# Kernel tuning notes

Measured on AMD Instinct MI355X. Metric: run time of the kernel, lower is better.

The kernel has to match this reference:

```python
import jax, jax.numpy as jnp
import numpy as np

C = 256      # channels (multiple of 32 for GroupNorm)
K = 3        # kernel
PAD = 1      # padding
G = 32       # GroupNorm groups
EPS = 1e-5


def setup_inputs() -> dict:
    key = jax.random.key(0)
    ks = jax.random.split(key, 7)
    B, H, W = 4, 64, 64
    return {
        "x": jax.random.normal(ks[0], (B, C, H, W), jnp.float32),
        "offset": jax.random.normal(ks[1], (B, 2 * K * K, H, W), jnp.float32),
        "weight": jax.random.normal(ks[2], (C, C, K, K), jnp.float32) * 0.01,
        "att_w": jax.random.normal(ks[3], (1, C), jnp.float32) * 0.01,
        "att_b": jnp.zeros((1,), jnp.float32),
        "gamma": jnp.ones((C,), jnp.float32),
        "beta": jnp.zeros((C,), jnp.float32),
    }


def _bilinear_one(xb, py, px):
    # xb: [C, H, W]; py, px: [KK, H, W] fractional sample coords (zero-pad outside)
    H, W = xb.shape[1], xb.shape[2]
    y0 = jnp.floor(py)
    x0 = jnp.floor(px)
    y1 = y0 + 1.0
    x1 = x0 + 1.0
    wy1 = py - y0
    wy0 = 1.0 - wy1
    wx1 = px - x0
    wx0 = 1.0 - wx1

    def g(yi, xi):
        valid = (yi >= 0) & (yi < H) & (xi >= 0) & (xi < W)
        yc = jnp.clip(yi, 0, H - 1).astype(jnp.int32)
        xc = jnp.clip(xi, 0, W - 1).astype(jnp.int32)
        return xb[:, yc, xc] * valid[None].astype(xb.dtype)  # [C, KK, H, W]

    return (g(y0, x0) * (wy0 * wx0)[None] + g(y0, x1) * (wy0 * wx1)[None]
            + g(y1, x0) * (wy1 * wx0)[None] + g(y1, x1) * (wy1 * wx1)[None])


def reference(x, offset, weight, att_w, att_b, gamma, beta):
    B, Cc, H, W = x.shape
    KK = K * K
    off = offset.reshape(B, KK, 2, H, W)  # (dy, dx) per kernel tap
    ii, jj = jnp.meshgrid(jnp.arange(K), jnp.arange(K), indexing='ij')
    dky = (ii - PAD).reshape(KK).astype(x.dtype)
    dkx = (jj - PAD).reshape(KK).astype(x.dtype)
    ys = jnp.arange(H, dtype=x.dtype)
    xs = jnp.arange(W, dtype=x.dtype)
    # sample coords [B, KK, H, W]
    py = ys[None, :, None] + dky[:, None, None] + off[:, :, 0]
    px = xs[None, None, :] + dkx[:, None, None] + off[:, :, 1]

    # deformable unfold: [B, C, KK, H, W]
    xu = jax.vmap(_bilinear_one)(x, py, px)

    # max over kernel taps -> channel attention gate
    xm = xu.max(axis=2)  # [B, C, H, W]
    att = jax.nn.sigmoid(jnp.einsum('bchw,oc->bohw', xm, att_w)
                         + att_b[None, :, None, None])  # [B, 1, H, W]

    # gate the unfolded samples, then emulate the conv as one GEMM
    xw = xu * att[:, :, None]  # broadcast over C, KK
    cols = xw.transpose(1, 2, 0, 3, 4).reshape(Cc * KK, B * H * W)  # [C*KK, BHW]
    out = (weight.reshape(Cc, Cc * KK) @ cols).reshape(Cc, B, H, W).transpose(1, 0, 2, 3)

    # GroupNorm(32, C) + ReLU
    og = out.reshape(B, G, Cc // G, H, W)
    mu = og.mean(axis=(2, 3, 4), keepdims=True)
    var = og.var(axis=(2, 3, 4), keepdims=True)
    on = ((og - mu) * jax.lax.rsqrt(var + EPS)).reshape(B, Cc, H, W)
    return jax.nn.relu(on * gamma[None, :, None, None] + beta[None, :, None, None])
```

## Files before the change

### kernel.cpp

```cpp
#include <hip/hip_runtime.h>

#define CT 256
#define KDIM 2304
#define COLP 296
#define CCOL (32 * COLP)
#define XSP 4608

typedef unsigned short u16;
typedef _Float16 h2 __attribute__((ext_vector_type(2)));
typedef _Float16 h8 __attribute__((ext_vector_type(8)));
typedef __attribute__((ext_vector_type(4))) float f32x4;

__device__ __forceinline__ unsigned pkh(float a, float b) {
    h2 r; r[0] = (_Float16)a; r[1] = (_Float16)b;
    return __builtin_bit_cast(unsigned, r);
}

__device__ __forceinline__ void gload_lds16(const uint4* g, u16* l) {
    __builtin_amdgcn_global_load_lds((const __attribute__((address_space(1))) void*)g,
                                     (__attribute__((address_space(3))) void*)l, 16, 0, 0);
}

__global__ __launch_bounds__(256) void k_prep(const float* __restrict__ x, uint4* __restrict__ xi,
                                              const float* __restrict__ wgt, uint4* __restrict__ pw)
{
    if (blockIdx.x < 2048) {
        int u = blockIdx.x * 256 + threadIdx.x;
        int bcg = u >> 12, p = u & 4095;
        const float* xp = x + (((size_t)bcg) << 15) + p;
        unsigned r[4];
#pragma unroll
        for (int i = 0; i < 4; ++i)
            r[i] = pkh(xp[(size_t)(2 * i) << 12], xp[(size_t)(2 * i + 1) << 12]);
        uint4 o; o.x = r[0]; o.y = r[1]; o.z = r[2]; o.w = r[3];
        xi[u] = o;
    } else {
        int u = (blockIdx.x - 2048) * 256 + threadIdx.x;
        int kc = u >> 10, rm = u & 1023;
        int m = rm >> 2, j = rm & 3;
        int round = kc / 9, tap = kc - round * 9;
        const float* src = wgt + (size_t)m * KDIM + tap;
        int c0 = round * 32 + j * 8;
        unsigned q[4];
#pragma unroll
        for (int i = 0; i < 4; ++i)
            q[i] = pkh(src[(size_t)(c0 + 2 * i) * 9], src[(size_t)(c0 + 2 * i + 1) * 9]);
        uint4 o; o.x = q[0]; o.y = q[1]; o.z = q[2]; o.w = q[3];
        pw[u] = o;
    }
}

__device__ __forceinline__ void gather_one(int it2, int sp, int xsb, size_t gfall,
                                           const uint2* s_wt, const int2* s_off,
                                           const u16* Xs, u16* col,
                                           const uint4* __restrict__ xi, int rbase, int nw)
{
    int tap = it2 >> 5, nn = it2 & 31;
    uint2 wp = s_wt[it2];
    h2 w01 = __builtin_bit_cast(h2, wp.x);
    h2 w23 = __builtin_bit_cast(h2, wp.y);
    h2 wxp = (h2){w01[0], w01[0]}, wyp = (h2){w01[1], w01[1]};
    h2 wzp = (h2){w23[0], w23[0]}, wwp = (h2){w23[1], w23[1]};
    int2 of = s_off[it2];
    int P00 = of.x & 0xffff, P01 = (of.x >> 16) & 0xffff;
    int P10 = of.y & 0xffff, P11 = (of.y >> 16) & 0xffff;
    uint4 c00, c01, c10, c11;
    int Q;
    Q = P00 - rbase;
    if ((unsigned)Q < (unsigned)nw) c00 = *(const uint4*)&Xs[xsb + Q * 8]; else c00 = xi[gfall + P00];
    Q = P01 - rbase;
    if ((unsigned)Q < (unsigned)nw) c01 = *(const uint4*)&Xs[xsb + Q * 8]; else c01 = xi[gfall + P01];
    Q = P10 - rbase;
    if ((unsigned)Q < (unsigned)nw) c10 = *(const uint4*)&Xs[xsb + Q * 8]; else c10 = xi[gfall + P10];
    Q = P11 - rbase;
    if ((unsigned)Q < (unsigned)nw) c11 = *(const uint4*)&Xs[xsb + Q * 8]; else c11 = xi[gfall + P11];
    const unsigned* a00 = (const unsigned*)&c00;
    const unsigned* a01 = (const unsigned*)&c01;
    const unsigned* a10 = (const unsigned*)&c10;
    const unsigned* a11 = (const unsigned*)&c11;
    unsigned o[4];
#pragma unroll
    for (int q = 0; q < 4; ++q) {
        h2 r = wxp * __builtin_bit_cast(h2, a00[q]) + wyp * __builtin_bit_cast(h2, a01[q])
             + wzp * __builtin_bit_cast(h2, a10[q]) + wwp * __builtin_bit_cast(h2, a11[q]);
        o[q] = __builtin_bit_cast(unsigned, r);
    }
    uint4 ov; ov.x = o[0]; ov.y = o[1]; ov.z = o[2]; ov.w = o[3];
    *(uint4*)&col[nn * COLP + tap * 32 + sp * 8] = ov;
}

__global__ __launch_bounds__(512, 2) void k_main(const uint4* __restrict__ xi, const float* __restrict__ off,
                                                 const uint4* __restrict__ pw, const float* __restrict__ att_w,
                                                 const float* __restrict__ att_b,
                                                 float* __restrict__ outp, float* __restrict__ gnpart)
{
    __shared__ uint2 s_wt[288];
    __shared__ int2 s_off[288];
    __shared__ u16 Xs[4 * XSP];
    __shared__ u16 col[2 * CCOL];
    __shared__ float s_att[32];

    int bid = blockIdx.x;
    int xcd = bid & 7, idx = bid >> 3;
    int b = xcd >> 1;
    int local = ((xcd & 1) << 6) + idx;
    int h = local >> 1, half = local & 1;
    int lbid = b * 128 + local;
    int n0 = half * 32;

    int tid = threadIdx.x;
    int lane = tid & 63, w = tid >> 6;
    int l15 = lane & 15, kb = lane >> 4;
    int wm = w * 32;
    int nn_a = w * 4 + (lane >> 4);
    int ca = (lane & 15) * 2;

    for (int e = tid; e < 288; e += 512) {
        int kk = e >> 5, wl = e & 31;
        int ww_ = n0 + wl;
        int ky = kk / 3, kx = kk - ky * 3;
        float dy = off[((size_t)(b * 18 + 2 * kk) * 64 + h) * 64 + ww_];
        float dx = off[((size_t)(b * 18 + 2 * kk + 1) * 64 + h) * 64 + ww_];
        float py = (float)(h + ky - 1) + dy;
        float px = (float)(ww_ + kx - 1) + dx;
        float y0f = floorf(py), x0f = floorf(px);
        int y0 = (int)y0f, x0 = (int)x0f;
        float fy = py - y0f, fx = px - x0f;
        float vy0 = (y0 >= 0 && y0 < 64) ? 1.f : 0.f;
        float vy1 = (y0 >= -1 && y0 < 63) ? 1.f : 0.f;
        float vx0 = (x0 >= 0 && x0 < 64) ? 1.f : 0.f;
        float vx1 = (x0 >= -1 && x0 < 63) ? 1.f : 0.f;
        float w0 = (1.f - fy) * (1.f - fx) * vy0 * vx0;
        float w1 = (1.f - fy) * fx * vy0 * vx1;
        float w2 = fy * (1.f - fx) * vy1 * vx0;
        float w3 = fy * fx * vy1 * vx1;
        uint2 wp;
        wp.x = pkh(w0, w1);
        wp.y = pkh(w2, w3);
        int yc0 = min(max(y0, 0), 63), yc1 = min(max(y0 + 1, 0), 63);
        int xc0 = min(max(x0, 0), 63), xc1 = min(max(x0 + 1, 0), 63);
        s_wt[e] = wp;
        s_off[e] = make_int2((yc0 * 64 + xc0) | ((yc0 * 64 + xc1) << 16),
                             (yc1 * 64 + xc0) | ((yc1 * 64 + xc1) << 16));
    }

    int r0c = max(0, h - 4), r1c = min(63, h + 4);
    int nrows = r1c - r0c + 1, nw = nrows * 64, rbase = r0c * 64;
    size_t xib = (size_t)(b * 32) << 12;

    float att_acc = 0.f;
    f32x4 acc[2][2];
#pragma unroll
    for (int mt = 0; mt < 2; ++mt)
#pragma unroll
        for (int nt = 0; nt < 2; ++nt) acc[mt][nt] = (f32x4){0.f, 0.f, 0.f, 0.f};

    int pwoff[2];
#pragma unroll
    for (int mt = 0; mt < 2; ++mt) pwoff[mt] = (wm + mt * 16 + l15) * 4 + kb;

#pragma unroll
    for (int cgl = 0; cgl < 2; ++cgl)
        for (int e = tid; e < nw; e += 512)
            gload_lds16(&xi[xib + ((size_t)cgl << 12) + rbase + e], &Xs[(cgl * XSP + e * 8)]);

    for (int stage = 0; stage < 16; ++stage) {
        int buf = stage & 1;
        __syncthreads();
        if (stage < 15) {
            size_t nb = xib + ((size_t)((stage + 1) * 2) << 12) + rbase;
#pragma unroll
            for (int cgl = 0; cgl < 2; ++cgl)
                for (int e = tid; e < nw; e += 512)
                    gload_lds16(&xi[nb + ((size_t)cgl << 12) + e],
                                &Xs[(((buf ^ 1) * 2 + cgl) * XSP + e * 8)]);
        }

        if (stage >= 2 && !(stage & 1)) {
            int rr = (stage >> 1) - 1;
            const u16* cb = col + (rr & 1) * CCOL;

            uint4 aa[4][2];
#pragma unroll
            for (int ts = 0; ts < 4; ++ts)
#pragma unroll
                for (int mt = 0; mt < 2; ++mt)
                    aa[ts][mt] = pw[(size_t)(rr * 9 + ts) * 1024 + pwoff[mt]];

            {
                int sp = ca >> 3, co = ca & 7;
                const u16* base = &cb[nn_a * COLP + sp * 8 + co];
                float m0 = -1e30f, m1 = -1e30f;
#pragma unroll
                for (int t = 0; t < 9; ++t) {
                    unsigned v = *(const unsigned*)(base + t * 32);
                    h2 vv = __builtin_bit_cast(h2, v);
                    m0 = fmaxf(m0, (float)vv[0]);
                    m1 = fmaxf(m1, (float)vv[1]);
                }
                int cbx = rr * 32 + ca;
                att_acc += att_w[cbx] * m0 + att_w[cbx + 1] * m1;
            }

#pragma unroll
            for (int ts = 0; ts < 9; ++ts) {
                h8 bf[2];
#pragma unroll
                for (int nt = 0; nt < 2; ++nt)
                    bf[nt] = *(const h8*)&cb[(nt * 16 + l15) * COLP + ts * 32 + kb * 8];
                h8 af[2];
#pragma unroll
                for (int mt = 0; mt < 2; ++mt) af[mt] = __builtin_bit_cast(h8, aa[ts & 3][mt]);
                if (ts + 4 < 9) {
#pragma unroll
                    for (int mt = 0; mt < 2; ++mt)
                        aa[ts & 3][mt] = pw[(size_t)(rr * 9 + ts + 4) * 1024 + pwoff[mt]];
                }
#pragma unroll
                for (int mt = 0; mt < 2; ++mt)
#pragma unroll
                    for (int nt = 0; nt < 2; ++nt)
                        acc[mt][nt] = __builtin_amdgcn_mfma_f32_16x16x32_f16(af[mt], bf[nt], acc[mt][nt], 0, 0, 0);
            }
        }

        {
            u16* cw = col + ((stage >> 1) & 1) * CCOL;
            int it = tid;
            int cgl = (it >= 288) ? 1 : 0;
            gather_one(it - cgl * 288, buf * 2 + cgl, (buf * 2 + cgl) * XSP,
                       xib + ((size_t)(stage * 2 + cgl) << 12), s_wt, s_off, Xs, cw, xi, rbase, nw);
            if (tid >= 448) {
                int it2 = tid + 64;
                gather_one(it2 - 288, buf * 2 + 1, (buf * 2 + 1) * XSP,
                           xib + ((size_t)(stage * 2 + 1) << 12), s_wt, s_off, Xs, cw, xi, rbase, nw);
            }
        }
    }

    __syncthreads();
    {
        int rr = 7;
        const u16* cb = col + (rr & 1) * CCOL;
        uint4 aa[4][2];
#pragma unroll
        for (int ts = 0; ts < 4; ++ts)
#pragma unroll
            for (int mt = 0; mt < 2; ++mt)
                aa[ts][mt] = pw[(size_t)(rr * 9 + ts) * 1024 + pwoff[mt]];
        {
            int sp = ca >> 3, co = ca & 7;
            const u16* base = &cb[nn_a * COLP + sp * 8 + co];
            float m0 = -1e30f, m1 = -1e30f;
#pragma unroll
            for (int t = 0; t < 9; ++t) {
                unsigned v = *(const unsigned*)(base + t * 32);
                h2 vv = __builtin_bit_cast(h2, v);
                m0 = fmaxf(m0, (float)vv[0]);
                m1 = fmaxf(m1, (float)vv[1]);
            }
            int cbx = rr * 32 + ca;
            att_acc += att_w[cbx] * m0 + att_w[cbx + 1] * m1;
        }
#pragma unroll
        for (int ts = 0; ts < 9; ++ts) {
            h8 bf[2];
#pragma unroll
            for (int nt = 0; nt < 2; ++nt)
                bf[nt] = *(const h8*)&cb[(nt * 16 + l15) * COLP + ts * 32 + kb * 8];
            h8 af[2];
#pragma unroll
            for (int mt = 0; mt < 2; ++mt) af[mt] = __builtin_bit_cast(h8, aa[ts & 3][mt]);
            if (ts + 4 < 9) {
#pragma unroll
                for (int mt = 0; mt < 2; ++mt)
                    aa[ts & 3][mt] = pw[(size_t)(rr * 9 + ts + 4) * 1024 + pwoff[mt]];
            }
#pragma unroll
            for (int mt = 0; mt < 2; ++mt)
#pragma unroll
                for (int nt = 0; nt < 2; ++nt)
                    acc[mt][nt] = __builtin_amdgcn_mfma_f32_16x16x32_f16(af[mt], bf[nt], acc[mt][nt], 0, 0, 0);
        }
    }

#pragma unroll
    for (int d = 1; d <= 8; d <<= 1) att_acc += __shfl_xor(att_acc, d);
    if ((lane & 15) == 0) s_att[nn_a] = 1.f / (1.f + expf(-(att_acc + att_b[0])));
    __syncthreads();

    float attn[2];
#pragma unroll
    for (int nt = 0; nt < 2; ++nt) attn[nt] = s_att[nt * 16 + l15];

#pragma unroll
    for (int mt = 0; mt < 2; ++mt) {
        float s1 = 0.f, s2 = 0.f;
#pragma unroll
        for (int nt = 0; nt < 2; ++nt)
#pragma unroll
            for (int r = 0; r < 4; ++r) {
                float v = acc[mt][nt][r] * attn[nt];
                int m = wm + mt * 16 + kb * 4 + r;
                outp[(((size_t)(b * CT + m)) << 12) + h * 64 + n0 + nt * 16 + l15] = v;
                s1 += v; s2 += v * v;
            }
#pragma unroll
        for (int d = 1; d <= 16; d <<= 1) {
            s1 += __shfl_xor(s1, d);
            s2 += __shfl_xor(s2, d);
        }
        if ((lane & 31) == 0) {
            int gidx = w * 4 + mt * 2 + (kb >> 1);
            gnpart[lbid * 64 + gidx * 2] = s1;
            gnpart[lbid * 64 + gidx * 2 + 1] = s2;
        }
    }
}

__global__ __launch_bounds__(256) void k_gn(const float* __restrict__ gnpart, const float* __restrict__ gamma,
                                            const float* __restrict__ beta, float* __restrict__ outp)
{
    __shared__ float rs1[128], rs2[128];
    __shared__ float s_stat[2];
    int bg = blockIdx.x;
    int b = bg >> 5, g = bg & 31;
    int tid = threadIdx.x;
    if (tid < 128) {
        int blk = (b * 64 + (tid >> 1)) * 2 + (tid & 1);
        rs1[tid] = gnpart[blk * 64 + g * 2];
        rs2[tid] = gnpart[blk * 64 + g * 2 + 1];
    }
    __syncthreads();
    if (tid < 64) {
        float a = rs1[tid] + rs1[tid + 64];
        float c = rs2[tid] + rs2[tid + 64];
#pragma unroll
        for (int d = 1; d <= 32; d <<= 1) {
            a += __shfl_xor(a, d);
            c += __shfl_xor(c, d);
        }
        if (tid == 0) {
            float mean = a * (1.f / 32768.f);
            float var = c * (1.f / 32768.f) - mean * mean;
            s_stat[0] = mean;
            s_stat[1] = rsqrtf(var + 1e-5f);
        }
    }
    __syncthreads();
    float mean = s_stat[0], rstd = s_stat[1];
    float4* p4 = (float4*)(outp + ((size_t)(b * CT + g * 8) << 12));
    for (int i = tid; i < 8192; i += 256) {
        int c = g * 8 + (i >> 10);
        float ga = gamma[c], be = beta[c];
        float4 v = p4[i];
        float4 r;
        r.x = fmaxf((v.x - mean) * rstd * ga + be, 0.f);
        r.y = fmaxf((v.y - mean) * rstd * ga + be, 0.f);
        r.z = fmaxf((v.z - mean) * rstd * ga + be, 0.f);
        r.w = fmaxf((v.w - mean) * rstd * ga + be, 0.f);
        p4[i] = r;
    }
}

extern "C" void kernel_launch(void* const* d_in, const int* in_sizes, int n_in,
                              void* d_out, int out_size, void* d_ws, size_t ws_size,
                              hipStream_t stream)
{
    const float* x = (const float*)d_in[0];
    const float* off = (const float*)d_in[1];
    const float* wgt = (const float*)d_in[2];
    const float* attw = (const float*)d_in[3];
    const float* attb = (const float*)d_in[4];
    const float* gamma = (const float*)d_in[5];
    const float* beta = (const float*)d_in[6];
    float* outp = (float*)d_out;

    char* ws = (char*)d_ws;
    uint4* xi = (uint4*)ws;
    uint4* pw = (uint4*)(ws + 8388608);
    float* gnpart = (float*)(ws + 9568256);

    k_prep<<<dim3(2336), dim3(256), 0, stream>>>(x, xi, wgt, pw);
    k_main<<<dim3(512), dim3(512), 0, stream>>>(xi, off, pw, attw, attb, outp, gnpart);
    k_gn<<<dim3(128), dim3(256), 0, stream>>>(gnpart, gamma, beta, outp);
}
```

Before: 146.0 us.

## Fuse prep, main and GroupNorm into one cooperative kernel with grid syncs

```diff
diff --git a/kernel.cpp b/kernel.cpp
--- a/kernel.cpp
+++ b/kernel.cpp
@@ -1,10 +1,14 @@
 #include <hip/hip_runtime.h>
+#include <hip/hip_cooperative_groups.h>
+
+namespace cg = cooperative_groups;
 
 #define CT 256
 #define KDIM 2304
 #define COLP 296
 #define CCOL (32 * COLP)
-#define XSP 4608
+#define XSPB 4608
+#define XSPF 3584
 
 typedef unsigned short u16;
 typedef _Float16 h2 __attribute__((ext_vector_type(2)));
@@ -19,35 +23,6 @@
 __device__ __forceinline__ void gload_lds16(const uint4* g, u16* l) {
     __builtin_amdgcn_global_load_lds((const __attribute__((address_space(1))) void*)g,
                                      (__attribute__((address_space(3))) void*)l, 16, 0, 0);
-}
-
-__global__ __launch_bounds__(256) void k_prep(const float* __restrict__ x, uint4* __restrict__ xi,
-                                              const float* __restrict__ wgt, uint4* __restrict__ pw)
-{
-    if (blockIdx.x < 2048) {
-        int u = blockIdx.x * 256 + threadIdx.x;
-        int bcg = u >> 12, p = u & 4095;
-        const float* xp = x + (((size_t)bcg) << 15) + p;
-        unsigned r[4];
-#pragma unroll
-        for (int i = 0; i < 4; ++i)
-            r[i] = pkh(xp[(size_t)(2 * i) << 12], xp[(size_t)(2 * i + 1) << 12]);
-        uint4 o; o.x = r[0]; o.y = r[1]; o.z = r[2]; o.w = r[3];
-        xi[u] = o;
-    } else {
-        int u = (blockIdx.x - 2048) * 256 + threadIdx.x;
-        int kc = u >> 10, rm = u & 1023;
-        int m = rm >> 2, j = rm & 3;
-        int round = kc / 9, tap = kc - round * 9;
-        const float* src = wgt + (size_t)m * KDIM + tap;
-        int c0 = round * 32 + j * 8;
-        unsigned q[4];
-#pragma unroll
-        for (int i = 0; i < 4; ++i)
-            q[i] = pkh(src[(size_t)(c0 + 2 * i) * 9], src[(size_t)(c0 + 2 * i + 1) * 9]);
-        uint4 o; o.x = q[0]; o.y = q[1]; o.z = q[2]; o.w = q[3];
-        pw[u] = o;
-    }
 }
 
 __device__ __forceinline__ void gather_one(int it2, int sp, int xsb, size_t gfall,
@@ -89,16 +64,21 @@
     *(uint4*)&col[nn * COLP + tap * 32 + sp * 8] = ov;
 }
 
-__global__ __launch_bounds__(512, 2) void k_main(const uint4* __restrict__ xi, const float* __restrict__ off,
-                                                 const uint4* __restrict__ pw, const float* __restrict__ att_w,
-                                                 const float* __restrict__ att_b,
-                                                 float* __restrict__ outp, float* __restrict__ gnpart)
+__global__ __launch_bounds__(512, 2) void k_all(
+    const float* __restrict__ x, uint4* __restrict__ xi,
+    const float* __restrict__ wgt, uint4* __restrict__ pw,
+    const float* __restrict__ off, const float* __restrict__ att_w,
+    const float* __restrict__ att_b, const float* __restrict__ gamma,
+    const float* __restrict__ beta, float* __restrict__ outp,
+    float* __restrict__ gnpart, float* __restrict__ gstat)
 {
     __shared__ uint2 s_wt[288];
     __shared__ int2 s_off[288];
-    __shared__ u16 Xs[4 * XSP];
-    __shared__ u16 col[2 * CCOL];
+    __shared__ __align__(16) u16 Xs[4 * XSPF];
+    __shared__ __align__(16) u16 col[2 * CCOL];
     __shared__ float s_att[32];
+
+    cg::grid_group grid = cg::this_grid();
 
     int bid = blockIdx.x;
     int xcd = bid & 7, idx = bid >> 3;
@@ -114,6 +94,35 @@
     int wm = w * 32;
     int nn_a = w * 4 + (lane >> 4);
     int ca = (lane & 15) * 2;
+
+    {
+        int gthr = bid * 512 + tid;
+#pragma unroll
+        for (int rep = 0; rep < 2; ++rep) {
+            int u = gthr + rep * 262144;
+            int bcg = u >> 12, p = u & 4095;
+            const float* xp = x + (((size_t)bcg) << 15) + p;
+            unsigned rr[4];
+#pragma unroll
+            for (int i = 0; i < 4; ++i)
+                rr[i] = pkh(xp[(size_t)(2 * i) << 12], xp[(size_t)(2 * i + 1) << 12]);
+            uint4 o; o.x = rr[0]; o.y = rr[1]; o.z = rr[2]; o.w = rr[3];
+            xi[u] = o;
+        }
+        if (gthr < 73728) {
+            int kc = gthr >> 10, rm = gthr & 1023;
+            int m = rm >> 2, j = rm & 3;
+            int round = kc / 9, tap = kc - round * 9;
+            const float* src = wgt + (size_t)m * KDIM + tap;
+            int c0 = round * 32 + j * 8;
+            unsigned q[4];
+#pragma unroll
+            for (int i = 0; i < 4; ++i)
+                q[i] = pkh(src[(size_t)(c0 + 2 * i) * 9], src[(size_t)(c0 + 2 * i + 1) * 9]);
+            uint4 o; o.x = q[0]; o.y = q[1]; o.z = q[2]; o.w = q[3];
+            pw[gthr] = o;
+        }
+    }
 
     for (int e = tid; e < 288; e += 512) {
         int kk = e >> 5, wl = e & 31;
@@ -144,7 +153,7 @@
                              (yc1 * 64 + xc0) | ((yc1 * 64 + xc1) << 16));
     }
 
-    int r0c = max(0, h - 4), r1c = min(63, h + 4);
+    int r0c = max(0, h - 3), r1c = min(63, h + 3);
     int nrows = r1c - r0c + 1, nw = nrows * 64, rbase = r0c * 64;
     size_t xib = (size_t)(b * 32) << 12;
 
@@ -159,10 +168,13 @@
 #pragma unroll
     for (int mt = 0; mt < 2; ++mt) pwoff[mt] = (wm + mt * 16 + l15) * 4 + kb;
 
+    __threadfence();
+    grid.sync();
+
 #pragma unroll
     for (int cgl = 0; cgl < 2; ++cgl)
         for (int e = tid; e < nw; e += 512)
-            gload_lds16(&xi[xib + ((size_t)cgl << 12) + rbase + e], &Xs[(cgl * XSP + e * 8)]);
+            gload_lds16(&xi[xib + ((size_t)cgl << 12) + rbase + e], &Xs[(cgl * XSPF + e * 8)]);
 
     for (int stage = 0; stage < 16; ++stage) {
         int buf = stage & 1;
@@ -173,7 +185,7 @@
             for (int cgl = 0; cgl < 2; ++cgl)
                 for (int e = tid; e < nw; e += 512)
                     gload_lds16(&xi[nb + ((size_t)cgl << 12) + e],
-                                &Xs[(((buf ^ 1) * 2 + cgl) * XSP + e * 8)]);
+                                &Xs[(((buf ^ 1) * 2 + cgl) * XSPF + e * 8)]);
         }
 
         if (stage >= 2 && !(stage & 1)) {
@@ -228,11 +240,314 @@
             u16* cw = col + ((stage >> 1) & 1) * CCOL;
             int it = tid;
             int cgl = (it >= 288) ? 1 : 0;
-            gather_one(it - cgl * 288, buf * 2 + cgl, (buf * 2 + cgl) * XSP,
+            gather_one(it - cgl * 288, buf * 2 + cgl, (buf * 2 + cgl) * XSPF,
                        xib + ((size_t)(stage * 2 + cgl) << 12), s_wt, s_off, Xs, cw, xi, rbase, nw);
             if (tid >= 448) {
                 int it2 = tid + 64;
-                gather_one(it2 - 288, buf * 2 + 1, (buf * 2 + 1) * XSP,
+                gather_one(it2 - 288, buf * 2 + 1, (buf * 2 + 1) * XSPF,
+                           xib + ((size_t)(stage * 2 + 1) << 12), s_wt, s_off, Xs, cw, xi, rbase, nw);
+            }
+        }
+    }
+
+    __syncthreads();
+    {
+        int rr = 7;
+        const u16* cb = col + (rr & 1) * CCOL;
+        uint4 aa[4][2];
+#pragma unroll
+        for (int ts = 0; ts < 4; ++ts)
+#pragma unroll
+            for (int mt = 0; mt < 2; ++mt)
+                aa[ts][mt] = pw[(size_t)(rr * 9 + ts) * 1024 + pwoff[mt]];
+        {
+            int sp = ca >> 3, co = ca & 7;
+            const u16* base = &cb[nn_a * COLP + sp * 8 + co];
+            float m0 = -1e30f, m1 = -1e30f;
+#pragma unroll
+            for (int t = 0; t < 9; ++t) {
+                unsigned v = *(const unsigned*)(base + t * 32);
+                h2 vv = __builtin_bit_cast(h2, v);
+                m0 = fmaxf(m0, (float)vv[0]);
+                m1 = fmaxf(m1, (float)vv[1]);
+            }
+            int cbx = rr * 32 + ca;
+            att_acc += att_w[cbx] * m0 + att_w[cbx + 1] * m1;
+        }
+#pragma unroll
+        for (int ts = 0; ts < 9; ++ts) {
+            h8 bf[2];
+#pragma unroll
+            for (int nt = 0; nt < 2; ++nt)
+                bf[nt] = *(const h8*)&cb[(nt * 16 + l15) * COLP + ts * 32 + kb * 8];
+            h8 af[2];
+#pragma unroll
+            for (int mt = 0; mt < 2; ++mt) af[mt] = __builtin_bit_cast(h8, aa[ts & 3][mt]);
+            if (ts + 4 < 9) {
+#pragma unroll
+                for (int mt = 0; mt < 2; ++mt)
+                    aa[ts & 3][mt] = pw[(size_t)(rr * 9 + ts + 4) * 1024 + pwoff[mt]];
+            }
+#pragma unroll
+            for (int mt = 0; mt < 2; ++mt)
+#pragma unroll
+                for (int nt = 0; nt < 2; ++nt)
+                    acc[mt][nt] = __builtin_amdgcn_mfma_f32_16x16x32_f16(af[mt], bf[nt], acc[mt][nt], 0, 0, 0);
+        }
+    }
+
+#pragma unroll
+    for (int d = 1; d <= 8; d <<= 1) att_acc += __shfl_xor(att_acc, d);
+    if ((lane & 15) == 0) s_att[nn_a] = 1.f / (1.f + expf(-(att_acc + att_b[0])));
+    __syncthreads();
+
+    float attn[2];
+#pragma unroll
+    for (int nt = 0; nt < 2; ++nt) attn[nt] = s_att[nt * 16 + l15];
+
+#pragma unroll
+    for (int mt = 0; mt < 2; ++mt) {
+        float s1 = 0.f, s2 = 0.f;
+#pragma unroll
+        for (int nt = 0; nt < 2; ++nt)
+#pragma unroll
+            for (int r = 0; r < 4; ++r) {
+                float v = acc[mt][nt][r] * attn[nt];
+                acc[mt][nt][r] = v;
+                s1 += v; s2 += v * v;
+            }
+#pragma unroll
+        for (int d = 1; d <= 16; d <<= 1) {
+            s1 += __shfl_xor(s1, d);
+            s2 += __shfl_xor(s2, d);
+        }
+        if ((lane & 31) == 0) {
+            int gidx = w * 4 + mt * 2 + (kb >> 1);
+            gnpart[lbid * 64 + gidx * 2] = s1;
+            gnpart[lbid * 64 + gidx * 2 + 1] = s2;
+        }
+    }
+
+    __threadfence();
+    grid.sync();
+
+    if (bid < 128) {
+        int b2 = bid >> 5, g2 = bid & 31;
+        float* rs = (float*)col;
+        if (tid < 128) {
+            rs[tid]       = gnpart[(size_t)(b2 * 128 + tid) * 64 + g2 * 2];
+            rs[tid + 128] = gnpart[(size_t)(b2 * 128 + tid) * 64 + g2 * 2 + 1];
+        }
+        __syncthreads();
+        if (tid < 64) {
+            float a = rs[tid] + rs[tid + 64];
+            float c = rs[tid + 128] + rs[tid + 192];
+#pragma unroll
+            for (int d = 1; d <= 32; d <<= 1) {
+                a += __shfl_xor(a, d);
+                c += __shfl_xor(c, d);
+            }
+            if (tid == 0) {
+                float mean = a * (1.f / 32768.f);
+                float var = c * (1.f / 32768.f) - mean * mean;
+                gstat[(b2 * 32 + g2) * 2] = mean;
+                gstat[(b2 * 32 + g2) * 2 + 1] = rsqrtf(var + 1e-5f);
+            }
+        }
+    }
+
+    __threadfence();
+    grid.sync();
+
+#pragma unroll
+    for (int mt = 0; mt < 2; ++mt) {
+        int gg = ((wm + mt * 16) >> 3) + (kb >> 1);
+        float mean = gstat[(b * 32 + gg) * 2];
+        float rstd = gstat[(b * 32 + gg) * 2 + 1];
+#pragma unroll
+        for (int r = 0; r < 4; ++r) {
+            int m = wm + mt * 16 + kb * 4 + r;
+            float ga = gamma[m], be = beta[m];
+#pragma unroll
+            for (int nt = 0; nt < 2; ++nt) {
+                float v = acc[mt][nt][r];
+                float o = fmaxf((v - mean) * rstd * ga + be, 0.f);
+                outp[(((size_t)(b * CT + m)) << 12) + h * 64 + n0 + nt * 16 + l15] = o;
+            }
+        }
+    }
+}
+
+__global__ __launch_bounds__(256) void k_prep(const float* __restrict__ x, uint4* __restrict__ xi,
+                                              const float* __restrict__ wgt, uint4* __restrict__ pw)
+{
+    if (blockIdx.x < 2048) {
+        int u = blockIdx.x * 256 + threadIdx.x;
+        int bcg = u >> 12, p = u & 4095;
+        const float* xp = x + (((size_t)bcg) << 15) + p;
+        unsigned r[4];
+#pragma unroll
+        for (int i = 0; i < 4; ++i)
+            r[i] = pkh(xp[(size_t)(2 * i) << 12], xp[(size_t)(2 * i + 1) << 12]);
+        uint4 o; o.x = r[0]; o.y = r[1]; o.z = r[2]; o.w = r[3];
+        xi[u] = o;
+    } else {
+        int u = (blockIdx.x - 2048) * 256 + threadIdx.x;
+        int kc = u >> 10, rm = u & 1023;
+        int m = rm >> 2, j = rm & 3;
+        int round = kc / 9, tap = kc - round * 9;
+        const float* src = wgt + (size_t)m * KDIM + tap;
+        int c0 = round * 32 + j * 8;
+        unsigned q[4];
+#pragma unroll
+        for (int i = 0; i < 4; ++i)
+            q[i] = pkh(src[(size_t)(c0 + 2 * i) * 9], src[(size_t)(c0 + 2 * i + 1) * 9]);
+        uint4 o; o.x = q[0]; o.y = q[1]; o.z = q[2]; o.w = q[3];
+        pw[u] = o;
+    }
+}
+
+__global__ __launch_bounds__(512, 2) void k_main(const uint4* __restrict__ xi, const float* __restrict__ off,
+                                                 const uint4* __restrict__ pw, const float* __restrict__ att_w,
+                                                 const float* __restrict__ att_b,
+                                                 float* __restrict__ outp, float* __restrict__ gnpart)
+{
+    __shared__ uint2 s_wt[288];
+    __shared__ int2 s_off[288];
+    __shared__ u16 Xs[4 * XSPB];
+    __shared__ u16 col[2 * CCOL];
+    __shared__ float s_att[32];
+
+    int bid = blockIdx.x;
+    int xcd = bid & 7, idx = bid >> 3;
+    int b = xcd >> 1;
+    int local = ((xcd & 1) << 6) + idx;
+    int h = local >> 1, half = local & 1;
+    int lbid = b * 128 + local;
+    int n0 = half * 32;
+
+    int tid = threadIdx.x;
+    int lane = tid & 63, w = tid >> 6;
+    int l15 = lane & 15, kb = lane >> 4;
+    int wm = w * 32;
+    int nn_a = w * 4 + (lane >> 4);
+    int ca = (lane & 15) * 2;
+
+    for (int e = tid; e < 288; e += 512) {
+        int kk = e >> 5, wl = e & 31;
+        int ww_ = n0 + wl;
+        int ky = kk / 3, kx = kk - ky * 3;
+        float dy = off[((size_t)(b * 18 + 2 * kk) * 64 + h) * 64 + ww_];
+        float dx = off[((size_t)(b * 18 + 2 * kk + 1) * 64 + h) * 64 + ww_];
+        float py = (float)(h + ky - 1) + dy;
+        float px = (float)(ww_ + kx - 1) + dx;
+        float y0f = floorf(py), x0f = floorf(px);
+        int y0 = (int)y0f, x0 = (int)x0f;
+        float fy = py - y0f, fx = px - x0f;
+        float vy0 = (y0 >= 0 && y0 < 64) ? 1.f : 0.f;
+        float vy1 = (y0 >= -1 && y0 < 63) ? 1.f : 0.f;
+        float vx0 = (x0 >= 0 && x0 < 64) ? 1.f : 0.f;
+        float vx1 = (x0 >= -1 && x0 < 63) ? 1.f : 0.f;
+        float w0 = (1.f - fy) * (1.f - fx) * vy0 * vx0;
+        float w1 = (1.f - fy) * fx * vy0 * vx1;
+        float w2 = fy * (1.f - fx) * vy1 * vx0;
+        float w3 = fy * fx * vy1 * vx1;
+        uint2 wp;
+        wp.x = pkh(w0, w1);
+        wp.y = pkh(w2, w3);
+        int yc0 = min(max(y0, 0), 63), yc1 = min(max(y0 + 1, 0), 63);
+        int xc0 = min(max(x0, 0), 63), xc1 = min(max(x0 + 1, 0), 63);
+        s_wt[e] = wp;
+        s_off[e] = make_int2((yc0 * 64 + xc0) | ((yc0 * 64 + xc1) << 16),
+                             (yc1 * 64 + xc0) | ((yc1 * 64 + xc1) << 16));
+    }
+
+    int r0c = max(0, h - 4), r1c = min(63, h + 4);
+    int nrows = r1c - r0c + 1, nw = nrows * 64, rbase = r0c * 64;
+    size_t xib = (size_t)(b * 32) << 12;
+
+    float att_acc = 0.f;
+    f32x4 acc[2][2];
+#pragma unroll
+    for (int mt = 0; mt < 2; ++mt)
+#pragma unroll
+        for (int nt = 0; nt < 2; ++nt) acc[mt][nt] = (f32x4){0.f, 0.f, 0.f, 0.f};
+
+    int pwoff[2];
+#pragma unroll
+    for (int mt = 0; mt < 2; ++mt) pwoff[mt] = (wm + mt * 16 + l15) * 4 + kb;
+
+#pragma unroll
+    for (int cgl = 0; cgl < 2; ++cgl)
+        for (int e = tid; e < nw; e += 512)
+            gload_lds16(&xi[xib + ((size_t)cgl << 12) + rbase + e], &Xs[(cgl * XSPB + e * 8)]);
+
+    for (int stage = 0; stage < 16; ++stage) {
+        int buf = stage & 1;
+        __syncthreads();
+        if (stage < 15) {
+            size_t nb = xib + ((size_t)((stage + 1) * 2) << 12) + rbase;
+#pragma unroll
+            for (int cgl = 0; cgl < 2; ++cgl)
+                for (int e = tid; e < nw; e += 512)
+                    gload_lds16(&xi[nb + ((size_t)cgl << 12) + e],
+                                &Xs[(((buf ^ 1) * 2 + cgl) * XSPB + e * 8)]);
+        }
+
+        if (stage >= 2 && !(stage & 1)) {
+            int rr = (stage >> 1) - 1;
+            const u16* cb = col + (rr & 1) * CCOL;
+            uint4 aa[4][2];
+#pragma unroll
+            for (int ts = 0; ts < 4; ++ts)
+#pragma unroll
+                for (int mt = 0; mt < 2; ++mt)
+                    aa[ts][mt] = pw[(size_t)(rr * 9 + ts) * 1024 + pwoff[mt]];
+            {
+                int sp = ca >> 3, co = ca & 7;
+                const u16* base = &cb[nn_a * COLP + sp * 8 + co];
+                float m0 = -1e30f, m1 = -1e30f;
+#pragma unroll
+                for (int t = 0; t < 9; ++t) {
+                    unsigned v = *(const unsigned*)(base + t * 32);
+                    h2 vv = __builtin_bit_cast(h2, v);
+                    m0 = fmaxf(m0, (float)vv[0]);
+                    m1 = fmaxf(m1, (float)vv[1]);
+                }
+                int cbx = rr * 32 + ca;
+                att_acc += att_w[cbx] * m0 + att_w[cbx + 1] * m1;
+            }
+#pragma unroll
+            for (int ts = 0; ts < 9; ++ts) {
+                h8 bf[2];
+#pragma unroll
+                for (int nt = 0; nt < 2; ++nt)
+                    bf[nt] = *(const h8*)&cb[(nt * 16 + l15) * COLP + ts * 32 + kb * 8];
+                h8 af[2];
+#pragma unroll
+                for (int mt = 0; mt < 2; ++mt) af[mt] = __builtin_bit_cast(h8, aa[ts & 3][mt]);
+                if (ts + 4 < 9) {
+#pragma unroll
+                    for (int mt = 0; mt < 2; ++mt)
+                        aa[ts & 3][mt] = pw[(size_t)(rr * 9 + ts + 4) * 1024 + pwoff[mt]];
+                }
+#pragma unroll
+                for (int mt = 0; mt < 2; ++mt)
+#pragma unroll
+                    for (int nt = 0; nt < 2; ++nt)
+                        acc[mt][nt] = __builtin_amdgcn_mfma_f32_16x16x32_f16(af[mt], bf[nt], acc[mt][nt], 0, 0, 0);
+            }
+        }
+
+        {
+            u16* cw = col + ((stage >> 1) & 1) * CCOL;
+            int it = tid;
+            int cgl = (it >= 288) ? 1 : 0;
+            gather_one(it - cgl * 288, buf * 2 + cgl, (buf * 2 + cgl) * XSPB,
+                       xib + ((size_t)(stage * 2 + cgl) << 12), s_wt, s_off, Xs, cw, xi, rbase, nw);
+            if (tid >= 448) {
+                int it2 = tid + 64;
+                gather_one(it2 - 288, buf * 2 + 1, (buf * 2 + 1) * XSPB,
                            xib + ((size_t)(stage * 2 + 1) << 12), s_wt, s_off, Xs, cw, xi, rbase, nw);
             }
         }
@@ -380,8 +695,16 @@
     uint4* xi = (uint4*)ws;
     uint4* pw = (uint4*)(ws + 8388608);
     float* gnpart = (float*)(ws + 9568256);
-
-    k_prep<<<dim3(2336), dim3(256), 0, stream>>>(x, xi, wgt, pw);
-    k_main<<<dim3(512), dim3(512), 0, stream>>>(xi, off, pw, attw, attb, outp, gnpart);
-    k_gn<<<dim3(128), dim3(256), 0, stream>>>(gnpart, gamma, beta, outp);
+    float* gstat = (float*)ws;
+
+    void* args[] = {(void*)&x, (void*)&xi, (void*)&wgt, (void*)&pw, (void*)&off,
+                    (void*)&attw, (void*)&attb, (void*)&gamma, (void*)&beta,
+                    (void*)&outp, (void*)&gnpart, (void*)&gstat};
+    hipError_t e = hipLaunchCooperativeKernel((const void*)k_all, dim3(512), dim3(512),
+                                              args, 0, stream);
+    if (e != hipSuccess) {
+        k_prep<<<dim3(2336), dim3(256), 0, stream>>>(x, xi, wgt, pw);
+        k_main<<<dim3(512), dim3(512), 0, stream>>>(xi, off, pw, attw, attb, outp, gnpart);
+        k_gn<<<dim3(128), dim3(256), 0, stream>>>(gnpart, gamma, beta, outp);
+    }
 }
```

Measured after the change: 547.1 us. +274.8%, slower.
